# Optimization experiments

Measured on AMD Instinct MI355X. Metric: run time of the kernel, lower is better.

Reference implementation:

```python
import math
import jax, jax.numpy as jnp
import numpy as np

NQ = 4   # n_qubits
NL = 2   # n_layers
H = 16   # num_heads


def _apply_gate(state, gate, q, batched):
    """Apply a 1-qubit gate on wire q to batched state [N, 2**NQ]."""
    n = state.shape[0]
    left, right = 2 ** q, 2 ** (NQ - 1 - q)
    s = state.reshape(n, left, 2, right)
    eq = 'nab,nlbr->nlar' if batched else 'ab,nlbr->nlar'
    return jnp.einsum(eq, gate, s).reshape(n, 2 ** NQ)


def _rot(phi, theta, omega):
    """PennyLane Rot(phi, theta, omega) = RZ(omega) RY(theta) RZ(phi), 2x2 unitary."""
    c = jnp.cos(theta / 2).astype(jnp.complex64)
    s = jnp.sin(theta / 2).astype(jnp.complex64)
    ep = jnp.exp(-0.5j * (phi + omega).astype(jnp.complex64))
    em = jnp.exp(0.5j * (phi - omega).astype(jnp.complex64))
    m00 = ep * c
    m01 = -em * s
    m10 = jnp.conj(em) * s
    m11 = jnp.conj(ep) * c
    return jnp.stack([jnp.stack([m00, m01]), jnp.stack([m10, m11])])


def _cnot01(state):
    """CNOT with control wire 0, target wire 1 on [N, 16]."""
    n = state.shape[0]
    s = state.reshape(n, 2, 2, 2 ** (NQ - 2))
    s = jnp.stack([s[:, 0], s[:, 1, ::-1]], axis=1)
    return s.reshape(n, 2 ** NQ)


def _quantum_block(inputs, params):
    """Analytic state-vector simulation of the PennyLane circuit.

    inputs: [N, NQ] rotation angles (AngleEmbedding, default RX).
    params: [NL, NQ, 3] Rot parameters.
    Returns [N, NQ] Pauli-Z expectation values.
    """
    n = inputs.shape[0]
    state = jnp.zeros((n, 2 ** NQ), jnp.complex64).at[:, 0].set(1.0)
    # AngleEmbedding: RX(inputs[:, q]) on wire q
    for q in range(NQ):
        a = inputs[:, q] * 0.5
        c = jnp.cos(a).astype(jnp.complex64)
        s = (-1j) * jnp.sin(a).astype(jnp.complex64)
        gate = jnp.stack([jnp.stack([c, s], -1), jnp.stack([s, c], -1)], -2)  # [N,2,2]
        state = _apply_gate(state, gate, q, batched=True)
    # Variational layers
    for l in range(NL):
        for q in range(NQ):
            g = _rot(params[l, q, 0], params[l, q, 1], params[l, q, 2])
            state = _apply_gate(state, g, q, batched=False)
        state = _cnot01(state)
    probs = (jnp.abs(state) ** 2).reshape(n, 2, 2, 2, 2)
    z = jnp.array([1.0, -1.0], probs.dtype)
    letters = 'abcd'
    evs = [jnp.einsum(f'nabcd,{letters[i]}->n', probs, z) for i in range(NQ)]
    return jnp.stack(evs, axis=-1)


def reference(x, params, w_q, w_k, w_v, w_o):
    B, S, E = x.shape
    dk = E // H

    def proj(w):
        return (x @ w.T).reshape(B, S, H, dk).transpose(0, 2, 1, 3)  # [B,H,S,dk]

    q, k, v = proj(w_q), proj(w_k), proj(w_v)

    def inject(t):
        ang = t[..., :NQ].reshape(-1, NQ)
        ev = _quantum_block(ang, params).reshape(B, H, S, NQ).astype(t.dtype)
        return t.at[..., :NQ].set(ev)

    q, k, v = inject(q), inject(k), inject(v)
    scores = jnp.einsum('bhqd,bhkd->bhqk', q, k) / math.sqrt(dk)
    attn = jax.nn.softmax(scores, axis=-1)
    out = jnp.einsum('bhqk,bhkd->bhqd', attn, v)
    out = out.transpose(0, 2, 1, 3).reshape(B, S, E)
    return out @ w_o.T


def setup_inputs() -> dict:
    key = jax.random.key(0)
    ks = jax.random.split(key, 6)
    B, S, E = 2, 2048, 1024
    scale = 1.0 / math.sqrt(E)
    return {
        'x': jax.random.normal(ks[0], (B, S, E), jnp.float32),
        'params': jax.random.normal(ks[1], (NL, NQ, 3), jnp.float32),
        'w_q': jax.random.normal(ks[2], (E, E), jnp.float32) * scale,
        'w_k': jax.random.normal(ks[3], (E, E), jnp.float32) * scale,
        'w_v': jax.random.normal(ks[4], (E, E), jnp.float32) * scale,
        'w_o': jax.random.normal(ks[5], (E, E), jnp.float32) * scale,
    }
```

## Files before the change

### kernel.cpp

```cpp
#include <hip/hip_runtime.h>
#include <math.h>

#define BATCH 2
#define S_LEN 2048
#define E_DIM 1024
#define NHEAD 16
#define DK 64
#define NROWS (BATCH * S_LEN)

typedef _Float16 f16x8 __attribute__((ext_vector_type(8)));
typedef _Float16 f16x4 __attribute__((ext_vector_type(4)));
typedef float    f32x4 __attribute__((ext_vector_type(4)));

__device__ __forceinline__ void glds16(_Float16* lds, const _Float16* g) {
    __builtin_amdgcn_global_load_lds(
        (const __attribute__((address_space(1))) unsigned int*)g,
        (__attribute__((address_space(3))) unsigned int*)lds,
        16, 0, 0);
}

__global__ __launch_bounds__(256) void conv_all(
    const float* __restrict__ x,  const float* __restrict__ wq,
    const float* __restrict__ wk, const float* __restrict__ wv,
    const float* __restrict__ wo,
    _Float16* __restrict__ xh,  _Float16* __restrict__ wqh,
    _Float16* __restrict__ wkh, _Float16* __restrict__ wvh,
    _Float16* __restrict__ woh) {
    const int id = blockIdx.x;
    const float* src; _Float16* dst; int lid;
    if (id < 4096)      { src = x;  dst = xh;  lid = id; }
    else if (id < 5120) { src = wq; dst = wqh; lid = id - 4096; }
    else if (id < 6144) { src = wk; dst = wkh; lid = id - 5120; }
    else if (id < 7168) { src = wv; dst = wvh; lid = id - 6144; }
    else                { src = wo; dst = woh; lid = id - 7168; }
    const int i = lid * 256 + threadIdx.x;
    float4 v = ((const float4*)src)[i];
    f16x4 h;
    h[0] = (_Float16)v.x; h[1] = (_Float16)v.y;
    h[2] = (_Float16)v.z; h[3] = (_Float16)v.w;
    ((f16x4*)dst)[i] = h;
}

__device__ __forceinline__ void gemm_body(const _Float16* __restrict__ X,
                                          const _Float16* __restrict__ W,
                                          void* __restrict__ dstv, int mode,
                                          _Float16* smem) {
    const int tid  = threadIdx.x;
    const int lane = tid & 63;
    const int w    = tid >> 6;
    const int wy = w >> 1, wx = w & 1;
    const int l15 = lane & 15, quad = lane >> 4;
    const int sw  = l15 & 7;
    const int m0 = blockIdx.y * 128, c0 = blockIdx.x * 128;

    const int lrow = lane >> 3;
    const int gcol = ((lane & 7) ^ lrow) * 8;
    const _Float16* xg = X + (size_t)(m0 + w * 32 + lrow) * E_DIM + gcol;
    const _Float16* wg = W + (size_t)(c0 + w * 32 + lrow) * E_DIM + gcol;
    const int woff = (w * 32) * 64;

    f32x4 acc[4][4];
#pragma unroll
    for (int i = 0; i < 4; ++i)
#pragma unroll
        for (int j = 0; j < 4; ++j) acc[i][j] = 0.f;

#pragma unroll
    for (int c = 0; c < 4; ++c) {
        glds16(smem + woff + c * 512,        xg + (size_t)c * 8 * E_DIM);
        glds16(smem + 8192 + woff + c * 512, wg + (size_t)c * 8 * E_DIM);
    }
    __syncthreads();

    for (int t = 0; t < E_DIM / 64; ++t) {
        const int buf = t & 1;
        _Float16* Xs = smem + buf * 16384;
        _Float16* Ws = Xs + 8192;
        if (t < E_DIM / 64 - 1) {
            _Float16* Xn = smem + (buf ^ 1) * 16384;
            const int k0 = (t + 1) * 64;
#pragma unroll
            for (int c = 0; c < 4; ++c) {
                glds16(Xn + woff + c * 512,        xg + (size_t)c * 8 * E_DIM + k0);
                glds16(Xn + 8192 + woff + c * 512, wg + (size_t)c * 8 * E_DIM + k0);
            }
        }

#pragma unroll
        for (int ks = 0; ks < 2; ++ks) {
            f16x8 af[4], bf[4];
#pragma unroll
            for (int i = 0; i < 4; ++i) {
                const int pc = ((ks * 4 + quad) ^ sw) * 8;
                af[i] = *(const f16x8*)&Xs[(wy * 64 + i * 16 + l15) * 64 + pc];
                bf[i] = *(const f16x8*)&Ws[(wx * 64 + i * 16 + l15) * 64 + pc];
            }
#pragma unroll
            for (int i = 0; i < 4; ++i)
#pragma unroll
                for (int j = 0; j < 4; ++j)
                    acc[i][j] = __builtin_amdgcn_mfma_f32_16x16x32_f16(af[i], bf[j], acc[i][j], 0, 0, 0);
        }
        __syncthreads();
    }

    if (mode == 2) {
        _Float16* Ct = smem;
#pragma unroll
        for (int i = 0; i < 4; ++i)
#pragma unroll
            for (int j = 0; j < 4; ++j) {
                const int col  = wx * 64 + j * 16 + l15;
                const int rowb = wy * 64 + i * 16 + quad * 4;
                f16x4 pk;
#pragma unroll
                for (int r = 0; r < 4; ++r) pk[r] = (_Float16)acc[i][j][r];
                *(f16x4*)&Ct[col * 136 + rowb] = pk;
            }
        __syncthreads();
        const int b  = m0 >> 11;
        const int s0 = m0 & 2047;
#pragma unroll
        for (int it = 0; it < 8; ++it) {
            const int c   = it * 256 + tid;
            const int col = c >> 4;
            const int rc  = c & 15;
            f16x8 v = *(const f16x8*)&Ct[col * 136 + rc * 8];
            const int e = c0 + col, h = e >> 6, d = e & 63;
            *(f16x8*)((_Float16*)dstv + ((size_t)((b * NHEAD + h) * DK + d)) * S_LEN + s0 + rc * 8) = v;
        }
        return;
    }

#pragma unroll
    for (int i = 0; i < 4; ++i)
#pragma unroll
        for (int j = 0; j < 4; ++j)
#pragma unroll
            for (int r = 0; r < 4; ++r) {
                const int row = m0 + wy * 64 + i * 16 + quad * 4 + r;
                const int col = c0 + wx * 64 + j * 16 + l15;
                const int b = row >> 11, s = row & 2047;
                const int h = col >> 6,  d = col & 63;
                ((_Float16*)dstv)[(((size_t)(b * NHEAD + h) * S_LEN + s) * DK) + d] =
                    (_Float16)acc[i][j][r];
            }
}

__global__ __launch_bounds__(256, 2) void gemm_qkv(
    const _Float16* __restrict__ X,
    const _Float16* __restrict__ WQ, const _Float16* __restrict__ WK,
    const _Float16* __restrict__ WV,
    _Float16* __restrict__ Qh, _Float16* __restrict__ Kh,
    _Float16* __restrict__ VTh) {
    __shared__ __align__(16) _Float16 smem[2 * 16384];
    const int z = blockIdx.z;
    const _Float16* W = (z == 0) ? WQ : (z == 1) ? WK : WV;
    void* dst = (z == 0) ? (void*)Qh : (z == 1) ? (void*)Kh : (void*)VTh;
    gemm_body(X, W, dst, (z == 2) ? 2 : 1, smem);
}

__global__ __launch_bounds__(256, 3) void gemm_out2(const _Float16* __restrict__ X,
                                                    const _Float16* __restrict__ W,
                                                    float* __restrict__ dst) {
    __shared__ __align__(16) _Float16 smem[2 * 12288];

    const int tid  = threadIdx.x;
    const int lane = tid & 63;
    const int w    = tid >> 6;
    const int wy = w >> 1, wx = w & 1;
    const int l15 = lane & 15, quad = lane >> 4;
    const int sw  = l15 & 7;
    const int m0 = blockIdx.y * 128, c0 = blockIdx.x * 64;

    const int lrow = lane >> 3;
    const int gcol = ((lane & 7) ^ lrow) * 8;
    const _Float16* xg = X + (size_t)(m0 + w * 32 + lrow) * E_DIM + gcol;
    const _Float16* wg = W + (size_t)(c0 + w * 16 + lrow) * E_DIM + gcol;
    const int xoff = (w * 32) * 64;
    const int woff = (w * 16) * 64;

    f32x4 acc[4][2];
#pragma unroll
    for (int i = 0; i < 4; ++i)
#pragma unroll
        for (int j = 0; j < 2; ++j) acc[i][j] = 0.f;

#pragma unroll
    for (int c = 0; c < 4; ++c)
        glds16(smem + xoff + c * 512, xg + (size_t)c * 8 * E_DIM);
#pragma unroll
    for (int c = 0; c < 2; ++c)
        glds16(smem + 8192 + woff + c * 512, wg + (size_t)c * 8 * E_DIM);
    __syncthreads();

    for (int t = 0; t < E_DIM / 64; ++t) {
        const int buf = t & 1;
        _Float16* Xs = smem + buf * 12288;
        _Float16* Ws = Xs + 8192;
        if (t < E_DIM / 64 - 1) {
            _Float16* Xn = smem + (buf ^ 1) * 12288;
            const int k0 = (t + 1) * 64;
#pragma unroll
            for (int c = 0; c < 4; ++c)
                glds16(Xn + xoff + c * 512, xg + (size_t)c * 8 * E_DIM + k0);
#pragma unroll
            for (int c = 0; c < 2; ++c)
                glds16(Xn + 8192 + woff + c * 512, wg + (size_t)c * 8 * E_DIM + k0);
        }

#pragma unroll
        for (int ks = 0; ks < 2; ++ks) {
            f16x8 af[4], bf[2];
#pragma unroll
            for (int i = 0; i < 4; ++i) {
                const int pc = ((ks * 4 + quad) ^ sw) * 8;
                af[i] = *(const f16x8*)&Xs[(wy * 64 + i * 16 + l15) * 64 + pc];
            }
#pragma unroll
            for (int j = 0; j < 2; ++j) {
                const int pc = ((ks * 4 + quad) ^ sw) * 8;
                bf[j] = *(const f16x8*)&Ws[(wx * 32 + j * 16 + l15) * 64 + pc];
            }
#pragma unroll
            for (int i = 0; i < 4; ++i)
#pragma unroll
                for (int j = 0; j < 2; ++j)
                    acc[i][j] = __builtin_amdgcn_mfma_f32_16x16x32_f16(af[i], bf[j], acc[i][j], 0, 0, 0);
        }
        __syncthreads();
    }

#pragma unroll
    for (int i = 0; i < 4; ++i)
#pragma unroll
        for (int j = 0; j < 2; ++j)
#pragma unroll
            for (int r = 0; r < 4; ++r) {
                const int row = m0 + wy * 64 + i * 16 + quad * 4 + r;
                const int col = c0 + wx * 32 + j * 16 + l15;
                dst[(size_t)row * E_DIM + col] = acc[i][j][r];
            }
}

__device__ __forceinline__ void apply_gate(float ar[16], float ai[16], int stride,
                                           float g00r, float g00i, float g01r, float g01i,
                                           float g10r, float g10i, float g11r, float g11i) {
#pragma unroll
    for (int i0 = 0; i0 < 16; ++i0) {
        if (i0 & stride) continue;
        const int i1 = i0 + stride;
        const float s0r = ar[i0], s0i = ai[i0];
        const float s1r = ar[i1], s1i = ai[i1];
        ar[i0] = g00r * s0r - g00i * s0i + g01r * s1r - g01i * s1i;
        ai[i0] = g00r * s0i + g00i * s0r + g01r * s1i + g01i * s1r;
        ar[i1] = g10r * s0r - g10i * s0i + g11r * s1r - g11i * s1i;
        ai[i1] = g10r * s0i + g10i * s0r + g11r * s1i + g11i * s1r;
    }
}

__global__ __launch_bounds__(256) void quantum_inject(_Float16* __restrict__ Q,
                                                      _Float16* __restrict__ K,
                                                      _Float16* __restrict__ VT,
                                                      const float* __restrict__ params) {
    const int id = blockIdx.x * 256 + threadIdx.x;
    const int which = id >> 16;
    const int rem = id & 65535;

    float angv[4];
    _Float16* qkbase = nullptr;
    _Float16* vbase  = nullptr;
    if (which == 2) {
        const int bh = rem >> 11, s = rem & 2047;
        vbase = VT + ((size_t)bh * DK) * S_LEN + s;
#pragma unroll
        for (int d = 0; d < 4; ++d) angv[d] = (float)vbase[(size_t)d * S_LEN];
    } else {
        qkbase = (which == 0 ? Q : K) + (size_t)rem * DK;
        const f16x4 a4 = *(const f16x4*)qkbase;
#pragma unroll
        for (int d = 0; d < 4; ++d) angv[d] = (float)a4[d];
    }

    float ar[16], ai[16];
#pragma unroll
    for (int i = 0; i < 16; ++i) { ar[i] = 0.f; ai[i] = 0.f; }
    ar[0] = 1.f;

#pragma unroll
    for (int q = 0; q < 4; ++q) {
        float sh, ch;
        sincosf(0.5f * angv[q], &sh, &ch);
        apply_gate(ar, ai, 8 >> q, ch, 0.f, 0.f, -sh, 0.f, -sh, ch, 0.f);
    }

#pragma unroll
    for (int l = 0; l < 2; ++l) {
#pragma unroll
        for (int q = 0; q < 4; ++q) {
            const float* pp = params + (l * 4 + q) * 3;
            const float phi = pp[0], th = pp[1], om = pp[2];
            float st, ct, sa, ca, sb, cb;
            sincosf(0.5f * th, &st, &ct);
            sincosf(0.5f * (phi + om), &sa, &ca);
            sincosf(0.5f * (phi - om), &sb, &cb);
            apply_gate(ar, ai, 8 >> q,
                       ct * ca, -ct * sa,
                       -st * cb, -st * sb,
                       st * cb, -st * sb,
                       ct * ca, ct * sa);
        }
#pragma unroll
        for (int r = 0; r < 4; ++r) {
            float tr = ar[8 + r], ti = ai[8 + r];
            ar[8 + r] = ar[12 + r]; ai[8 + r] = ai[12 + r];
            ar[12 + r] = tr;        ai[12 + r] = ti;
        }
    }

    float ev[4] = {0.f, 0.f, 0.f, 0.f};
#pragma unroll
    for (int i = 0; i < 16; ++i) {
        const float p = ar[i] * ar[i] + ai[i] * ai[i];
        ev[0] += (i & 8) ? -p : p;
        ev[1] += (i & 4) ? -p : p;
        ev[2] += (i & 2) ? -p : p;
        ev[3] += (i & 1) ? -p : p;
    }
    if (which == 2) {
#pragma unroll
        for (int d = 0; d < 4; ++d) vbase[(size_t)d * S_LEN] = (_Float16)ev[d];
    } else {
        f16x4 o;
#pragma unroll
        for (int d = 0; d < 4; ++d) o[d] = (_Float16)ev[d];
        *(f16x4*)qkbase = o;
    }
}

__global__ __launch_bounds__(256, 3) void attn7(const _Float16* __restrict__ Q,
                                                const _Float16* __restrict__ K,
                                                const _Float16* __restrict__ VT,
                                                _Float16* __restrict__ ctx) {
    __shared__ __align__(16) _Float16 KVs[2][2][64 * 64];

    const int tid = threadIdx.x, lane = tid & 63, w = tid >> 6;
    const int l15 = lane & 15, quad = lane >> 4;
    const int sw  = l15 & 7;
    const int bh = blockIdx.y;
    const int qbase = blockIdx.x * 128 + w * 32;

    const _Float16* Qb = Q  + (size_t)bh * S_LEN * DK;
    const _Float16* Kb = K  + (size_t)bh * S_LEN * DK;
    const _Float16* Vb = VT + (size_t)bh * DK * S_LEN;

    const int lrow = lane >> 3;
    const int gcol = ((lane & 7) ^ lrow) * 8;
    const int sr0  = 32 * (w >> 1) + 8 * (lrow >> 2) + 4 * (w & 1) + (lrow & 3);
    const _Float16* kg = Kb + (size_t)sr0 * DK + gcol;
    const _Float16* vg = Vb + (size_t)(w * 16 + lrow) * S_LEN + gcol;

    f16x8 bf[2][2];
#pragma unroll
    for (int qn = 0; qn < 2; ++qn)
#pragma unroll
        for (int ks = 0; ks < 2; ++ks)
            bf[qn][ks] = *(const f16x8*)(Qb + (size_t)(qbase + qn * 16 + l15) * DK + ks * 32 + quad * 8);

    f32x4 oacc[4][2];
#pragma unroll
    for (int dt = 0; dt < 4; ++dt)
#pragma unroll
        for (int qn = 0; qn < 2; ++qn) oacc[dt][qn] = 0.f;
    float lpart[2] = {0.f, 0.f};

#pragma unroll
    for (int c = 0; c < 2; ++c) {
        glds16(&KVs[0][0][(w * 16 + c * 8) * 64], kg + (size_t)(c * 16) * DK);
        glds16(&KVs[0][1][(w * 16 + c * 8) * 64], vg + (size_t)(c * 8) * S_LEN);
    }
    __syncthreads();

    for (int t = 0; t < S_LEN / 64; ++t) {
        const int buf = t & 1;
        if (t < S_LEN / 64 - 1) {
            const int kt = (t + 1) * 64;
#pragma unroll
            for (int c = 0; c < 2; ++c) {
                glds16(&KVs[buf ^ 1][0][(w * 16 + c * 8) * 64],
                       kg + (size_t)(kt + c * 16) * DK);
                glds16(&KVs[buf ^ 1][1][(w * 16 + c * 8) * 64],
                       vg + (size_t)(c * 8) * S_LEN + kt);
            }
        }

        f16x8 af[4][2], vt[4][2];
#pragma unroll
        for (int kc = 0; kc < 4; ++kc)
#pragma unroll
            for (int ks = 0; ks < 2; ++ks)
                af[kc][ks] = *(const f16x8*)&KVs[buf][0][(kc * 16 + l15) * 64 + ((ks * 4 + quad) ^ sw) * 8];
#pragma unroll
        for (int dt = 0; dt < 4; ++dt)
#pragma unroll
            for (int kh = 0; kh < 2; ++kh)
                vt[dt][kh] = *(const f16x8*)&KVs[buf][1][(dt * 16 + l15) * 64 + ((kh * 4 + quad) ^ sw) * 8];

        f16x4 pk4s[4][2];
#pragma unroll
        for (int kc = 0; kc < 4; ++kc)
#pragma unroll
            for (int qn = 0; qn < 2; ++qn) {
                f32x4 st = 0.f;
                st = __builtin_amdgcn_mfma_f32_16x16x32_f16(af[kc][0], bf[qn][0], st, 0, 0, 0);
                st = __builtin_amdgcn_mfma_f32_16x16x32_f16(af[kc][1], bf[qn][1], st, 0, 0, 0);
                float ps = 0.f;
                f16x4 pk;
#pragma unroll
                for (int r = 0; r < 4; ++r) {
                    const float p = __builtin_amdgcn_exp2f(
                        fmaf(st[r], 0.18033688011f, -4.32808512267f));
                    ps += p;
                    pk[r] = (_Float16)p;
                }
                lpart[qn] += ps;
                pk4s[kc][qn] = pk;
            }

#pragma unroll
        for (int dt = 0; dt < 4; ++dt)
#pragma unroll
            for (int qn = 0; qn < 2; ++qn)
#pragma unroll
                for (int kh = 0; kh < 2; ++kh) {
                    const f16x8 pb = __builtin_shufflevector(
                        pk4s[2 * kh][qn], pk4s[2 * kh + 1][qn],
                        0, 1, 2, 3, 4, 5, 6, 7);
                    oacc[dt][qn] = __builtin_amdgcn_mfma_f32_16x16x32_f16(
                        vt[dt][kh], pb, oacc[dt][qn], 0, 0, 0);
                }

        __syncthreads();
    }

    float inv[2];
#pragma unroll
    for (int qn = 0; qn < 2; ++qn) {
        float l = lpart[qn];
        l += __shfl_xor(l, 16);
        l += __shfl_xor(l, 32);
        inv[qn] = 1.f / l;
    }

    _Float16* ep = &KVs[0][0][0] + w * (32 * 72);
#pragma unroll
    for (int dt = 0; dt < 4; ++dt)
#pragma unroll
        for (int qn = 0; qn < 2; ++qn) {
            f16x4 ov;
#pragma unroll
            for (int r = 0; r < 4; ++r) ov[r] = (_Float16)(oacc[dt][qn][r] * inv[qn]);
            *(f16x4*)&ep[(qn * 16 + l15) * 72 + dt * 16 + quad * 4] = ov;
        }

    const int b = bh >> 4, h = bh & 15;
#pragma unroll
    for (int i = 0; i < 4; ++i) {
        const int c = i * 64 + lane;
        const int row = c >> 3, c8 = c & 7;
        f16x8 v = *(const f16x8*)&ep[row * 72 + c8 * 8];
        *(f16x8*)(ctx + (size_t)(b * S_LEN + qbase + row) * E_DIM + h * DK + c8 * 8) = v;
    }
}

extern "C" void kernel_launch(void* const* d_in, const int* in_sizes, int n_in,
                              void* d_out, int out_size, void* d_ws, size_t ws_size,
                              hipStream_t stream) {
    const float* x      = (const float*)d_in[0];
    const float* params = (const float*)d_in[1];
    const float* w_q    = (const float*)d_in[2];
    const float* w_k    = (const float*)d_in[3];
    const float* w_v    = (const float*)d_in[4];
    const float* w_o    = (const float*)d_in[5];
    float* out = (float*)d_out;

    const size_t TENS = (size_t)NROWS * E_DIM;
    const size_t WEL  = (size_t)E_DIM * E_DIM;
    _Float16* xh  = (_Float16*)d_ws;
    _Float16* wqh = xh  + TENS;
    _Float16* wkh = wqh + WEL;
    _Float16* wvh = wkh + WEL;
    _Float16* woh = wvh + WEL;
    _Float16* Qh  = woh + WEL;
    _Float16* Kh  = Qh  + TENS;
    _Float16* VTh = Kh  + TENS;
    _Float16* CTXh= VTh + TENS;

    dim3 blk(256);

    conv_all<<<dim3(8192), blk, 0, stream>>>(x, w_q, w_k, w_v, w_o,
                                             xh, wqh, wkh, wvh, woh);

    gemm_qkv<<<dim3(E_DIM / 128, NROWS / 128, 3), blk, 0, stream>>>(
        xh, wqh, wkh, wvh, Qh, Kh, VTh);

    quantum_inject<<<dim3(768), blk, 0, stream>>>(Qh, Kh, VTh, params);

    attn7<<<dim3(S_LEN / 128, BATCH * NHEAD), blk, 0, stream>>>(Qh, Kh, VTh, CTXh);

    gemm_out2<<<dim3(E_DIM / 64, NROWS / 128), blk, 0, stream>>>(CTXh, woh, out);
}
```

Baseline: 190.3 us.

## Triple-buffer attention K/V loads and fold softmax scale into K projection

The attention kernel moves from double to triple buffering of K/V tiles in LDS. It issues loads two tiles ahead and waits on vmcnt counters instead of a full __syncthreads. The softmax scale is pre-multiplied into K in the QKV GEMM epilogue and quantum injection, and the bias is folded into the MFMA accumulator init, which removes an FMA per score. The price is more LDS per block (48KB), which may lower occupancy, plus fp16 rounding of the scaled K.

```diff
diff --git a/kernel.cpp b/kernel.cpp
--- a/kernel.cpp
+++ b/kernel.cpp
@@ -7,6 +7,10 @@
 #define NHEAD 16
 #define DK 64
 #define NROWS (BATCH * S_LEN)
+
+#define SM_A    0.18033688011f
+#define SM_INVA 5.5451774444795623f
+#define SM_B   -4.32808512267f
 
 typedef _Float16 f16x8 __attribute__((ext_vector_type(8)));
 typedef _Float16 f16x4 __attribute__((ext_vector_type(4)));
@@ -44,7 +48,7 @@
 __device__ __forceinline__ void gemm_body(const _Float16* __restrict__ X,
                                           const _Float16* __restrict__ W,
                                           void* __restrict__ dstv, int mode,
-                                          _Float16* smem) {
+                                          float oscale, _Float16* smem) {
     const int tid  = threadIdx.x;
     const int lane = tid & 63;
     const int w    = tid >> 6;
@@ -114,7 +118,7 @@
                 const int rowb = wy * 64 + i * 16 + quad * 4;
                 f16x4 pk;
 #pragma unroll
-                for (int r = 0; r < 4; ++r) pk[r] = (_Float16)acc[i][j][r];
+                for (int r = 0; r < 4; ++r) pk[r] = (_Float16)(acc[i][j][r] * oscale);
                 *(f16x4*)&Ct[col * 136 + rowb] = pk;
             }
         __syncthreads();
@@ -143,7 +147,7 @@
                 const int b = row >> 11, s = row & 2047;
                 const int h = col >> 6,  d = col & 63;
                 ((_Float16*)dstv)[(((size_t)(b * NHEAD + h) * S_LEN + s) * DK) + d] =
-                    (_Float16)acc[i][j][r];
+                    (_Float16)(acc[i][j][r] * oscale);
             }
 }
 
@@ -157,7 +161,8 @@
     const int z = blockIdx.z;
     const _Float16* W = (z == 0) ? WQ : (z == 1) ? WK : WV;
     void* dst = (z == 0) ? (void*)Qh : (z == 1) ? (void*)Kh : (void*)VTh;
-    gemm_body(X, W, dst, (z == 2) ? 2 : 1, smem);
+    const float osc = (z == 1) ? SM_A : 1.0f;
+    gemm_body(X, W, dst, (z == 2) ? 2 : 1, osc, smem);
 }
 
 __global__ __launch_bounds__(256, 3) void gemm_out2(const _Float16* __restrict__ X,
@@ -278,8 +283,9 @@
     } else {
         qkbase = (which == 0 ? Q : K) + (size_t)rem * DK;
         const f16x4 a4 = *(const f16x4*)qkbase;
-#pragma unroll
-        for (int d = 0; d < 4; ++d) angv[d] = (float)a4[d];
+        const float asc = (which == 1) ? SM_INVA : 1.0f;
+#pragma unroll
+        for (int d = 0; d < 4; ++d) angv[d] = (float)a4[d] * asc;
     }
 
     float ar[16], ai[16];
@@ -331,18 +337,19 @@
 #pragma unroll
         for (int d = 0; d < 4; ++d) vbase[(size_t)d * S_LEN] = (_Float16)ev[d];
     } else {
+        const float osc = (which == 1) ? SM_A : 1.0f;
         f16x4 o;
 #pragma unroll
-        for (int d = 0; d < 4; ++d) o[d] = (_Float16)ev[d];
+        for (int d = 0; d < 4; ++d) o[d] = (_Float16)(ev[d] * osc);
         *(f16x4*)qkbase = o;
     }
 }
 
-__global__ __launch_bounds__(256, 3) void attn7(const _Float16* __restrict__ Q,
-                                                const _Float16* __restrict__ K,
-                                                const _Float16* __restrict__ VT,
-                                                _Float16* __restrict__ ctx) {
-    __shared__ __align__(16) _Float16 KVs[2][2][64 * 64];
+__global__ __launch_bounds__(256, 3) void attn10(const _Float16* __restrict__ Q,
+                                                 const _Float16* __restrict__ K,
+                                                 const _Float16* __restrict__ VT,
+                                                 _Float16* __restrict__ ctx) {
+    __shared__ __align__(16) _Float16 KVs[3][2][64 * 64];
 
     const int tid = threadIdx.x, lane = tid & 63, w = tid >> 6;
     const int l15 = lane & 15, quad = lane >> 4;
@@ -360,6 +367,16 @@
     const _Float16* kg = Kb + (size_t)sr0 * DK + gcol;
     const _Float16* vg = Vb + (size_t)(w * 16 + lrow) * S_LEN + gcol;
 
+    auto stage = [&](int u, int bidx) {
+        const int kt = u * 64;
+        _Float16* kb = &KVs[bidx][0][(w * 16) * 64];
+        _Float16* vb = &KVs[bidx][1][(w * 16) * 64];
+        glds16(kb,       kg + (size_t)kt * DK);
+        glds16(kb + 512, kg + (size_t)(kt + 16) * DK);
+        glds16(vb,       vg + (size_t)kt);
+        glds16(vb + 512, vg + (size_t)8 * S_LEN + kt);
+    };
+
     f16x8 bf[2][2];
 #pragma unroll
     for (int qn = 0; qn < 2; ++qn)
@@ -374,25 +391,14 @@
         for (int qn = 0; qn < 2; ++qn) oacc[dt][qn] = 0.f;
     float lpart[2] = {0.f, 0.f};
 
-#pragma unroll
-    for (int c = 0; c < 2; ++c) {
-        glds16(&KVs[0][0][(w * 16 + c * 8) * 64], kg + (size_t)(c * 16) * DK);
-        glds16(&KVs[0][1][(w * 16 + c * 8) * 64], vg + (size_t)(c * 8) * S_LEN);
-    }
-    __syncthreads();
-
+    stage(0, 0);
+    stage(1, 1);
+    asm volatile("s_waitcnt vmcnt(4)" ::: "memory");
+    __builtin_amdgcn_s_barrier();
+
+    int buf = 0, nbuf = 2;
     for (int t = 0; t < S_LEN / 64; ++t) {
-        const int buf = t & 1;
-        if (t < S_LEN / 64 - 1) {
-            const int kt = (t + 1) * 64;
-#pragma unroll
-            for (int c = 0; c < 2; ++c) {
-                glds16(&KVs[buf ^ 1][0][(w * 16 + c * 8) * 64],
-                       kg + (size_t)(kt + c * 16) * DK);
-                glds16(&KVs[buf ^ 1][1][(w * 16 + c * 8) * 64],
-                       vg + (size_t)(c * 8) * S_LEN + kt);
-            }
-        }
+        if (t < S_LEN / 64 - 2) stage(t + 2, nbuf);
 
         f16x8 af[4][2], vt[4][2];
 #pragma unroll
@@ -411,15 +417,14 @@
         for (int kc = 0; kc < 4; ++kc)
 #pragma unroll
             for (int qn = 0; qn < 2; ++qn) {
-                f32x4 st = 0.f;
+                f32x4 st = SM_B;
                 st = __builtin_amdgcn_mfma_f32_16x16x32_f16(af[kc][0], bf[qn][0], st, 0, 0, 0);
                 st = __builtin_amdgcn_mfma_f32_16x16x32_f16(af[kc][1], bf[qn][1], st, 0, 0, 0);
                 float ps = 0.f;
                 f16x4 pk;
 #pragma unroll
                 for (int r = 0; r < 4; ++r) {
-                    const float p = __builtin_amdgcn_exp2f(
-                        fmaf(st[r], 0.18033688011f, -4.32808512267f));
+                    const float p = __builtin_amdgcn_exp2f(st[r]);
                     ps += p;
                     pk[r] = (_Float16)p;
                 }
@@ -440,7 +445,15 @@
                         vt[dt][kh], pb, oacc[dt][qn], 0, 0, 0);
                 }
 
-        __syncthreads();
+        if (t < S_LEN / 64 - 2) {
+            asm volatile("s_waitcnt vmcnt(4)" ::: "memory");
+        } else if (t == S_LEN / 64 - 2) {
+            asm volatile("s_waitcnt vmcnt(0)" ::: "memory");
+        }
+        __builtin_amdgcn_s_barrier();
+
+        buf  = (buf == 2)  ? 0 : buf + 1;
+        nbuf = (nbuf == 2) ? 0 : nbuf + 1;
     }
 
     float inv[2];
@@ -506,7 +519,7 @@
 
     quantum_inject<<<dim3(768), blk, 0, stream>>>(Qh, Kh, VTh, params);
 
-    attn7<<<dim3(S_LEN / 128, BATCH * NHEAD), blk, 0, stream>>>(Qh, Kh, VTh, CTXh);
+    attn10<<<dim3(S_LEN / 128, BATCH * NHEAD), blk, 0, stream>>>(Qh, Kh, VTh, CTXh);
 
     gemm_out2<<<dim3(E_DIM / 64, NROWS / 128), blk, 0, stream>>>(CTXh, woh, out);
 }
```

Measured after the change: 187.9 us. Within noise of the previous version (-1.2%).
